# Kernel optimization log

Measured on AMD Instinct MI355X. Metric: run time of the kernel, lower is better.

Reference implementation:

```python
import jax, jax.numpy as jnp
import numpy as np

B, S, DIN, DOUT = 4, 2048, 4096, 4096

def setup_inputs() -> dict:
    key = jax.random.key(0)
    k1, k2, k3, k4 = jax.random.split(key, 4)
    x = jax.random.normal(k1, (B, S, DIN), dtype=jnp.float32)
    # int8-valued weights stored in int32 (harness dtype constraint); values in [-127, 127]
    weight_int8 = jax.random.randint(k2, (DOUT, DIN), -127, 128, dtype=jnp.int32)
    # per-output-channel scales, small positive values typical of int8 quantization
    scale = jax.random.uniform(k3, (DOUT,), dtype=jnp.float32, minval=1e-4, maxval=2e-2)
    bias = jax.random.normal(k4, (DOUT,), dtype=jnp.float32)
    return {"x": x, "weight_int8": weight_int8, "scale": scale, "bias": bias}

def reference(x, weight_int8, scale, bias):
    # Dequantize: w[o, i] = int8[o, i] * scale[o], cast to activation dtype
    w = (weight_int8.astype(jnp.float32) * scale[:, None]).astype(x.dtype)  # [DOUT, DIN]
    # F.linear: y = x @ w.T + bias
    return jnp.einsum('bsi,oi->bso', x, w) + bias
```

## Files before the change

### kernel.cpp

```cpp
#include <hip/hip_runtime.h>
#include <hip/hip_bf16.h>

#define BM 256
#define BN 256
#define BK 64
#define NSLOT 4

typedef float  f32x4  __attribute__((ext_vector_type(4)));
typedef int    i32x4  __attribute__((ext_vector_type(4)));
typedef int    i32x16 __attribute__((ext_vector_type(16)));
typedef __bf16 bf16x8 __attribute__((ext_vector_type(8)));
typedef __bf16 bf16x4 __attribute__((ext_vector_type(4)));

__device__ __forceinline__ void gload_lds16(const void* g, void* l) {
    __builtin_amdgcn_global_load_lds(
        (const __attribute__((address_space(1))) void*)g,
        (__attribute__((address_space(3))) void*)l, 16, 0, 0);
}

__global__ __launch_bounds__(256)
void rowquant_x(const float* __restrict__ x, signed char* __restrict__ xq,
                float* __restrict__ xs, int K) {
    const int row = blockIdx.x;
    const float* xr = x + (size_t)row * K;
    const int tid = threadIdx.x;
    const int n4 = K / 4;

    float mx = 0.f;
    for (int i = tid; i < n4; i += 256) {
        f32x4 v = ((const f32x4*)xr)[i];
        mx = fmaxf(mx, fmaxf(fmaxf(fabsf(v[0]), fabsf(v[1])),
                             fmaxf(fabsf(v[2]), fabsf(v[3]))));
    }
#pragma unroll
    for (int off = 32; off; off >>= 1)
        mx = fmaxf(mx, __shfl_xor(mx, off));
    __shared__ float smx[4];
    if ((tid & 63) == 0) smx[tid >> 6] = mx;
    __syncthreads();
    mx = fmaxf(fmaxf(smx[0], smx[1]), fmaxf(smx[2], smx[3]));

    const float inv = mx > 0.f ? 127.f / mx : 0.f;
    if (tid == 0) xs[row] = mx / 127.f;

    unsigned* out = (unsigned*)(xq + (size_t)row * K);
    for (int i = tid; i < n4; i += 256) {
        f32x4 v = ((const f32x4*)xr)[i];
        int q0 = __float2int_rn(v[0] * inv);
        int q1 = __float2int_rn(v[1] * inv);
        int q2 = __float2int_rn(v[2] * inv);
        int q3 = __float2int_rn(v[3] * inv);
        out[i] = (unsigned)(q0 & 255) | ((unsigned)(q1 & 255) << 8) |
                 ((unsigned)(q2 & 255) << 16) | ((unsigned)(q3 & 255) << 24);
    }
}

__global__ __launch_bounds__(256)
void cvt_w_i8(const int* __restrict__ w, unsigned* __restrict__ wq, int n4) {
    int i = blockIdx.x * 256 + threadIdx.x;
    const int stride = gridDim.x * 256;
    for (; i < n4; i += stride) {
        i32x4 v = ((const i32x4*)w)[i];
        wq[i] = (unsigned)(v[0] & 255) | ((unsigned)(v[1] & 255) << 8) |
                ((unsigned)(v[2] & 255) << 16) | ((unsigned)(v[3] & 255) << 24);
    }
}


__global__ __launch_bounds__(512, 2)
void qlin_gemm_i8(const signed char* __restrict__ A,
                  const signed char* __restrict__ B,
                  const float* __restrict__ xs,
                  const float* __restrict__ scale,
                  const float* __restrict__ bias,
                  float* __restrict__ C, int M, int N, int K) {
    extern __shared__ signed char lds[];
    signed char* lA = lds;
    signed char* lB = lds + NSLOT * (BM * BK);

    const int NTN = N / BN;
    const int nwg = gridDim.x;
    int bid = blockIdx.x;
    bid = (bid & 7) * (nwg >> 3) + (bid >> 3);
    const int tm = bid / NTN;
    const int tn = bid % NTN;

    const int tid  = threadIdx.x;
    const int lane = tid & 63;
    const int wid  = tid >> 6;
    const int wr   = wid >> 2;
    const int wc   = wid & 3;

    const int srow  = wid * 32 + (lane >> 1);
    const int shalf = (lane & 1) ^ ((srow >> 3) & 1);
    const signed char* Abase = A + (size_t)(tm * BM + srow) * K + shalf * 16;
    const signed char* Bbase = B + (size_t)(tn * BN + srow) * K + shalf * 16;

    const int NT = K / BK;

    auto STAGE_A = [&](int t) {
        signed char* d = lA + (t & (NSLOT - 1)) * (BM * BK) + wid * 1024;
#pragma unroll
        for (int j = 0; j < 2; ++j)
            gload_lds16(Abase + t * BK + j * 32, d + j * 8192);
    };
    auto STAGE_B = [&](int t) {
        signed char* d = lB + (t & (NSLOT - 1)) * (BM * BK) + wid * 1024;
#pragma unroll
        for (int j = 0; j < 2; ++j)
            gload_lds16(Bbase + t * BK + j * 32, d + j * 8192);
    };

    i32x16 acc[4][2];
#pragma unroll
    for (int mi = 0; mi < 4; ++mi)
#pragma unroll
        for (int ni = 0; ni < 2; ++ni)
#pragma unroll
            for (int r = 0; r < 16; ++r) acc[mi][ni][r] = 0;

    for (int u = 0; u < 3 && u < NT; ++u) { STAGE_A(u); STAGE_B(u); }

    const int fr = lane & 31;
    const int fh = lane >> 5;
    const int swz = (fr >> 3) & 1;

    for (int t = 0; t < NT; ++t) {
        const signed char* lAs = lA + (t & (NSLOT - 1)) * (BM * BK);
        const signed char* lBs = lB + (t & (NSLOT - 1)) * (BM * BK);

        const int rem = NT - 1 - t;
        if (rem >= 2)      asm volatile("s_waitcnt vmcnt(8)" ::: "memory");
        else if (rem == 1) asm volatile("s_waitcnt vmcnt(4)" ::: "memory");
        else               asm volatile("s_waitcnt vmcnt(0)" ::: "memory");
        __builtin_amdgcn_s_barrier();

        const int ho0 = ((fh ^ swz) << 4);
        const int ho1 = 8192 + ho0;
        i32x4 af0[4], af1[4], bf0[2], bf1[2];
#pragma unroll
        for (int mi = 0; mi < 4; ++mi) {
            const int R = wr * 128 + mi * 32 + fr;
            af0[mi] = *(const i32x4*)(lAs + R * 32 + ho0);
        }
#pragma unroll
        for (int ni = 0; ni < 2; ++ni) {
            const int R = wc * 64 + ni * 32 + fr;
            bf0[ni] = *(const i32x4*)(lBs + R * 32 + ho0);
        }
#pragma unroll
        for (int mi = 0; mi < 4; ++mi) {
            const int R = wr * 128 + mi * 32 + fr;
            af1[mi] = *(const i32x4*)(lAs + R * 32 + ho1);
        }
#pragma unroll
        for (int ni = 0; ni < 2; ++ni) {
            const int R = wc * 64 + ni * 32 + fr;
            bf1[ni] = *(const i32x4*)(lBs + R * 32 + ho1);
        }

        if (t + 3 < NT) { STAGE_A(t + 3); STAGE_B(t + 3); }

        __builtin_amdgcn_s_setprio(1);
#pragma unroll
        for (int mi = 0; mi < 4; ++mi)
#pragma unroll
            for (int ni = 0; ni < 2; ++ni)
                acc[mi][ni] = __builtin_amdgcn_mfma_i32_32x32x32_i8(
                    af0[mi], bf0[ni], acc[mi][ni], 0, 0, 0);
#pragma unroll
        for (int mi = 0; mi < 4; ++mi)
#pragma unroll
            for (int ni = 0; ni < 2; ++ni)
                acc[mi][ni] = __builtin_amdgcn_mfma_i32_32x32x32_i8(
                    af1[mi], bf1[ni], acc[mi][ni], 0, 0, 0);
        __builtin_amdgcn_s_setprio(0);
    }

    const int rb = tm * BM + wr * 128 + 4 * fh;
    const int cb = tn * BN + wc * 64 + fr;
#pragma unroll
    for (int mi = 0; mi < 4; ++mi) {
        float sm[16];
#pragma unroll
        for (int r = 0; r < 16; ++r)
            sm[r] = xs[rb + mi * 32 + (r & 3) + 8 * (r >> 2)];
#pragma unroll
        for (int ni = 0; ni < 2; ++ni) {
            const int n = cb + ni * 32;
            const float sc = scale[n];
            const float bs = bias[n];
#pragma unroll
            for (int r = 0; r < 16; ++r) {
                const int m = rb + mi * 32 + (r & 3) + 8 * (r >> 2);
                C[(size_t)m * N + n] = fmaf((float)acc[mi][ni][r], sm[r] * sc, bs);
            }
        }
    }
}

#define FBM 128
#define FBK 32

__device__ __forceinline__ int swz_elem(int row, int e) {
    return row * FBK + (e ^ (((row >> 1) & 3) << 3));
}

__global__ __launch_bounds__(256, 2)
void qlin_gemm_reg(const float* __restrict__ A, const int* __restrict__ W,
                   const float* __restrict__ scale, const float* __restrict__ bias,
                   float* __restrict__ C, int M, int N, int K) {
    __shared__ __bf16 lA[2][FBM * FBK];
    __shared__ __bf16 lB[2][FBM * FBK];
    const int NTN = N / FBM;
    const int nwg = gridDim.x;
    int bid = blockIdx.x;
    if ((nwg & 7) == 0) bid = (bid & 7) * (nwg >> 3) + (bid >> 3);
    const int tm = bid / NTN, tn = bid % NTN;
    const int tid = threadIdx.x, lane = tid & 63, wid = tid >> 6;
    const int wr = wid >> 1, wc = wid & 1;
    const int srow0 = tid >> 3, skq = tid & 7;
    const float* aptr = A + (size_t)(tm * FBM + srow0) * K + skq * 4;
    const int*   wptr = W + (size_t)(tn * FBM + srow0) * K + skq * 4;
    const size_t rstride = (size_t)32 * K;
    f32x4 sa[4]; i32x4 sw[4];
    auto LOAD = [&](int t) {
#pragma unroll
        for (int j = 0; j < 4; ++j) {
            sa[j] = *(const f32x4*)(aptr + (size_t)t * FBK + j * rstride);
            sw[j] = *(const i32x4*)(wptr + (size_t)t * FBK + j * rstride);
        }
    };
    auto STORE = [&](int buf) {
#pragma unroll
        for (int j = 0; j < 4; ++j) {
            const int idx = swz_elem(srow0 + j * 32, skq * 4);
            bf16x4 va = { (__bf16)sa[j][0], (__bf16)sa[j][1],
                          (__bf16)sa[j][2], (__bf16)sa[j][3] };
            bf16x4 vw = { (__bf16)(float)sw[j][0], (__bf16)(float)sw[j][1],
                          (__bf16)(float)sw[j][2], (__bf16)(float)sw[j][3] };
            *(bf16x4*)&lA[buf][idx] = va;
            *(bf16x4*)&lB[buf][idx] = vw;
        }
    };
    const f32x4 fzero = {0.f, 0.f, 0.f, 0.f};
    f32x4 acc[4][4];
#pragma unroll
    for (int i = 0; i < 4; ++i)
#pragma unroll
        for (int j = 0; j < 4; ++j) acc[i][j] = fzero;
    const int fr = lane & 15, fks = (lane >> 4) * 8;
    LOAD(0); STORE(0); __syncthreads();
    const int NT = K / FBK;
    for (int t = 0; t < NT; ++t) {
        const int buf = t & 1;
        if (t + 1 < NT) LOAD(t + 1);
        bf16x8 af[4], bfg[4];
#pragma unroll
        for (int mi = 0; mi < 4; ++mi)
            af[mi] = *(const bf16x8*)&lA[buf][swz_elem(wr * 64 + mi * 16 + fr, fks)];
#pragma unroll
        for (int ni = 0; ni < 4; ++ni)
            bfg[ni] = *(const bf16x8*)&lB[buf][swz_elem(wc * 64 + ni * 16 + fr, fks)];
#pragma unroll
        for (int mi = 0; mi < 4; ++mi)
#pragma unroll
            for (int ni = 0; ni < 4; ++ni)
                acc[mi][ni] = __builtin_amdgcn_mfma_f32_16x16x32_bf16(
                    af[mi], bfg[ni], acc[mi][ni], 0, 0, 0);
        if (t + 1 < NT) STORE(buf ^ 1);
        __syncthreads();
    }
    const int row0 = tm * FBM + wr * 64 + (lane >> 4) * 4;
    const int col0 = tn * FBM + wc * 64 + fr;
#pragma unroll
    for (int ni = 0; ni < 4; ++ni) {
        const int n = col0 + ni * 16;
        const float sc = scale[n], bs = bias[n];
#pragma unroll
        for (int mi = 0; mi < 4; ++mi) {
            const int m = row0 + mi * 16;
#pragma unroll
            for (int r = 0; r < 4; ++r)
                C[(size_t)(m + r) * N + n] = fmaf(acc[mi][ni][r], sc, bs);
        }
    }
}

extern "C" void kernel_launch(void* const* d_in, const int* in_sizes, int n_in,
                              void* d_out, int out_size, void* d_ws, size_t ws_size,
                              hipStream_t stream) {
    const float* x     = (const float*)d_in[0];
    const int*   w8    = (const int*)d_in[1];
    const float* scale = (const float*)d_in[2];
    const float* bias  = (const float*)d_in[3];
    float*       out   = (float*)d_out;

    const int DOUT = in_sizes[2];
    const int DIN  = in_sizes[1] / DOUT;
    const int M    = in_sizes[0] / DIN;

    const size_t need = (size_t)M * DIN + (size_t)DOUT * DIN + (size_t)M * 4;
    const int nwg = (M / BM) * (DOUT / BN);
    const bool ok = (ws_size >= need) && (M % BM == 0) && (DOUT % BN == 0) &&
                    (DIN % BK == 0) && (nwg % 8 == 0) && (DIN / BK >= 4);
    if (ok) {
        signed char* xq = (signed char*)d_ws;
        signed char* wq = xq + (size_t)M * DIN;
        float*       xs = (float*)(wq + (size_t)DOUT * DIN);
        rowquant_x<<<M, 256, 0, stream>>>(x, xq, xs, DIN);
        cvt_w_i8<<<2048, 256, 0, stream>>>(w8, (unsigned*)wq, DOUT * DIN / 4);
        hipFuncSetAttribute(reinterpret_cast<const void*>(qlin_gemm_i8),
                            hipFuncAttributeMaxDynamicSharedMemorySize, 131072);
        qlin_gemm_i8<<<nwg, 512, 131072, stream>>>(xq, wq, xs, scale, bias, out,
                                                   M, DOUT, DIN);
    } else {
        dim3 grid((M / FBM) * (DOUT / FBM));
        qlin_gemm_reg<<<grid, 256, 0, stream>>>(x, w8, scale, bias, out, M, DOUT, DIN);
    }
}
```

Baseline: 208.8 us.

## Switch int8 GEMM to 16x16x64 MFMA with row-contiguous swizzled LDS layout

Replaces the 32x32x32 int8 MFMA tiles with 16x16x64 int8 MFMA, so each wave now holds an 8x4 grid of 16x16 accumulators and issues one instruction per K-step of 64. The LDS staging layout changes from two 32-byte half-planes to full 64-byte rows with a 4-way XOR swizzle on 16-byte chunks, and the global-to-LDS loads are remapped to match. The aim is fewer LDS reads per tile, fewer bank conflicts and possibly higher MFMA throughput on this chip. The epilogue is rewritten for the new accumulator layout, which adds more scattered scalar loads of scale and bias and narrower output stores.

```diff
diff --git a/kernel.cpp b/kernel.cpp
--- a/kernel.cpp
+++ b/kernel.cpp
@@ -5,10 +5,10 @@
 #define BN 256
 #define BK 64
 #define NSLOT 4
+#define LDS_BYTES (2 * NSLOT * BM * BK)
 
 typedef float  f32x4  __attribute__((ext_vector_type(4)));
 typedef int    i32x4  __attribute__((ext_vector_type(4)));
-typedef int    i32x16 __attribute__((ext_vector_type(16)));
 typedef __bf16 bf16x8 __attribute__((ext_vector_type(8)));
 typedef __bf16 bf16x4 __attribute__((ext_vector_type(4)));
 
@@ -91,110 +91,98 @@
     const int wr   = wid >> 2;
     const int wc   = wid & 3;
 
-    const int srow  = wid * 32 + (lane >> 1);
-    const int shalf = (lane & 1) ^ ((srow >> 3) & 1);
-    const signed char* Abase = A + (size_t)(tm * BM + srow) * K + shalf * 16;
-    const signed char* Bbase = B + (size_t)(tn * BN + srow) * K + shalf * 16;
+    const int srow0 = wid * 32 + (lane >> 2);
+    const int srow1 = srow0 + 16;
+    const int gq0 = (lane & 3) ^ ((srow0 >> 1) & 3);
+    const int gq1 = (lane & 3) ^ ((srow1 >> 1) & 3);
+    const signed char* Ap0 = A + (size_t)(tm * BM + srow0) * K + gq0 * 16;
+    const signed char* Ap1 = A + (size_t)(tm * BM + srow1) * K + gq1 * 16;
+    const signed char* Bp0 = B + (size_t)(tn * BN + srow0) * K + gq0 * 16;
+    const signed char* Bp1 = B + (size_t)(tn * BN + srow1) * K + gq1 * 16;
 
     const int NT = K / BK;
 
     auto STAGE_A = [&](int t) {
-        signed char* d = lA + (t & (NSLOT - 1)) * (BM * BK) + wid * 1024;
-#pragma unroll
-        for (int j = 0; j < 2; ++j)
-            gload_lds16(Abase + t * BK + j * 32, d + j * 8192);
+        signed char* d = lA + (t & (NSLOT - 1)) * (BM * BK) + wid * 2048;
+        gload_lds16(Ap0 + t * BK, d);
+        gload_lds16(Ap1 + t * BK, d + 1024);
     };
     auto STAGE_B = [&](int t) {
-        signed char* d = lB + (t & (NSLOT - 1)) * (BM * BK) + wid * 1024;
-#pragma unroll
-        for (int j = 0; j < 2; ++j)
-            gload_lds16(Bbase + t * BK + j * 32, d + j * 8192);
-    };
-
-    i32x16 acc[4][2];
-#pragma unroll
-    for (int mi = 0; mi < 4; ++mi)
-#pragma unroll
-        for (int ni = 0; ni < 2; ++ni)
-#pragma unroll
-            for (int r = 0; r < 16; ++r) acc[mi][ni][r] = 0;
+        signed char* d = lB + (t & (NSLOT - 1)) * (BM * BK) + wid * 2048;
+        gload_lds16(Bp0 + t * BK, d);
+        gload_lds16(Bp1 + t * BK, d + 1024);
+    };
+
+    const int fr = lane & 15;
+    const int kq = lane >> 4;
+
+    auto AOFF = [&](int mi) {
+        const int R = wr * 128 + mi * 16 + fr;
+        return R * 64 + ((kq ^ ((R >> 1) & 3)) << 4);
+    };
+    auto BOFF = [&](int ni) {
+        const int R = wc * 64 + ni * 16 + fr;
+        return R * 64 + ((kq ^ ((R >> 1) & 3)) << 4);
+    };
+
+    i32x4 acc[8][4];
+#pragma unroll
+    for (int mi = 0; mi < 8; ++mi)
+#pragma unroll
+        for (int ni = 0; ni < 4; ++ni) {
+            acc[mi][ni][0] = 0; acc[mi][ni][1] = 0;
+            acc[mi][ni][2] = 0; acc[mi][ni][3] = 0;
+        }
 
     for (int u = 0; u < 3 && u < NT; ++u) { STAGE_A(u); STAGE_B(u); }
-
-    const int fr = lane & 31;
-    const int fh = lane >> 5;
-    const int swz = (fr >> 3) & 1;
 
     for (int t = 0; t < NT; ++t) {
         const signed char* lAs = lA + (t & (NSLOT - 1)) * (BM * BK);
         const signed char* lBs = lB + (t & (NSLOT - 1)) * (BM * BK);
-
         const int rem = NT - 1 - t;
+
         if (rem >= 2)      asm volatile("s_waitcnt vmcnt(8)" ::: "memory");
         else if (rem == 1) asm volatile("s_waitcnt vmcnt(4)" ::: "memory");
         else               asm volatile("s_waitcnt vmcnt(0)" ::: "memory");
         __builtin_amdgcn_s_barrier();
 
-        const int ho0 = ((fh ^ swz) << 4);
-        const int ho1 = 8192 + ho0;
-        i32x4 af0[4], af1[4], bf0[2], bf1[2];
-#pragma unroll
-        for (int mi = 0; mi < 4; ++mi) {
-            const int R = wr * 128 + mi * 32 + fr;
-            af0[mi] = *(const i32x4*)(lAs + R * 32 + ho0);
-        }
-#pragma unroll
-        for (int ni = 0; ni < 2; ++ni) {
-            const int R = wc * 64 + ni * 32 + fr;
-            bf0[ni] = *(const i32x4*)(lBs + R * 32 + ho0);
-        }
-#pragma unroll
-        for (int mi = 0; mi < 4; ++mi) {
-            const int R = wr * 128 + mi * 32 + fr;
-            af1[mi] = *(const i32x4*)(lAs + R * 32 + ho1);
-        }
-#pragma unroll
-        for (int ni = 0; ni < 2; ++ni) {
-            const int R = wc * 64 + ni * 32 + fr;
-            bf1[ni] = *(const i32x4*)(lBs + R * 32 + ho1);
-        }
+        i32x4 af[8], bf[4];
+#pragma unroll
+        for (int mi = 0; mi < 8; ++mi)
+            af[mi] = *(const i32x4*)(lAs + AOFF(mi));
+#pragma unroll
+        for (int ni = 0; ni < 4; ++ni)
+            bf[ni] = *(const i32x4*)(lBs + BOFF(ni));
 
         if (t + 3 < NT) { STAGE_A(t + 3); STAGE_B(t + 3); }
 
         __builtin_amdgcn_s_setprio(1);
 #pragma unroll
-        for (int mi = 0; mi < 4; ++mi)
-#pragma unroll
-            for (int ni = 0; ni < 2; ++ni)
-                acc[mi][ni] = __builtin_amdgcn_mfma_i32_32x32x32_i8(
-                    af0[mi], bf0[ni], acc[mi][ni], 0, 0, 0);
-#pragma unroll
-        for (int mi = 0; mi < 4; ++mi)
-#pragma unroll
-            for (int ni = 0; ni < 2; ++ni)
-                acc[mi][ni] = __builtin_amdgcn_mfma_i32_32x32x32_i8(
-                    af1[mi], bf1[ni], acc[mi][ni], 0, 0, 0);
+        for (int mi = 0; mi < 8; ++mi)
+#pragma unroll
+            for (int ni = 0; ni < 4; ++ni)
+                acc[mi][ni] = __builtin_amdgcn_mfma_i32_16x16x64_i8(
+                    af[mi], bf[ni], acc[mi][ni], 0, 0, 0);
         __builtin_amdgcn_s_setprio(0);
     }
 
-    const int rb = tm * BM + wr * 128 + 4 * fh;
+    const int rb = tm * BM + wr * 128 + (lane >> 4) * 4;
     const int cb = tn * BN + wc * 64 + fr;
 #pragma unroll
-    for (int mi = 0; mi < 4; ++mi) {
-        float sm[16];
-#pragma unroll
-        for (int r = 0; r < 16; ++r)
-            sm[r] = xs[rb + mi * 32 + (r & 3) + 8 * (r >> 2)];
-#pragma unroll
-        for (int ni = 0; ni < 2; ++ni) {
-            const int n = cb + ni * 32;
+    for (int mi = 0; mi < 8; ++mi) {
+        const int m0 = rb + mi * 16;
+        float sm[4];
+#pragma unroll
+        for (int r = 0; r < 4; ++r) sm[r] = xs[m0 + r];
+#pragma unroll
+        for (int ni = 0; ni < 4; ++ni) {
+            const int n = cb + ni * 16;
             const float sc = scale[n];
             const float bs = bias[n];
 #pragma unroll
-            for (int r = 0; r < 16; ++r) {
-                const int m = rb + mi * 32 + (r & 3) + 8 * (r >> 2);
-                C[(size_t)m * N + n] = fmaf((float)acc[mi][ni][r], sm[r] * sc, bs);
-            }
+            for (int r = 0; r < 4; ++r)
+                C[(size_t)(m0 + r) * N + n] =
+                    fmaf((float)acc[mi][ni][r], sm[r] * sc, bs);
         }
     }
 }
@@ -311,9 +299,9 @@
         rowquant_x<<<M, 256, 0, stream>>>(x, xq, xs, DIN);
         cvt_w_i8<<<2048, 256, 0, stream>>>(w8, (unsigned*)wq, DOUT * DIN / 4);
         hipFuncSetAttribute(reinterpret_cast<const void*>(qlin_gemm_i8),
-                            hipFuncAttributeMaxDynamicSharedMemorySize, 131072);
-        qlin_gemm_i8<<<nwg, 512, 131072, stream>>>(xq, wq, xs, scale, bias, out,
-                                                   M, DOUT, DIN);
+                            hipFuncAttributeMaxDynamicSharedMemorySize, LDS_BYTES);
+        qlin_gemm_i8<<<nwg, 512, LDS_BYTES, stream>>>(xq, wq, xs, scale, bias, out,
+                                                      M, DOUT, DIN);
     } else {
         dim3 grid((M / FBM) * (DOUT / FBM));
         qlin_gemm_reg<<<grid, 256, 0, stream>>>(x, w8, scale, bias, out, M, DOUT, DIN);
```

Measured after the change: 191.6 us (median of 2 runs). 1.09x faster.
